# Optimization experiments

Measured on AMD Instinct MI355X. Metric: run time of the kernel, lower is better.

Reference implementation:

```python
import jax, jax.numpy as jnp
import numpy as np
import math

NUM_HEADS = 16
D_MODEL = 1024
BATCH = 1
SEQ_LEN = 4096


def alibi_slopes(num_heads):
    # slopes m_h = (256 ** (1/H)) ** -(h+1)
    x = (2.0 ** 8) ** (1.0 / num_heads)
    return jnp.asarray([1.0 / x ** (i + 1) for i in range(num_heads)], dtype=jnp.float32)


def setup_inputs() -> dict:
    key = jax.random.key(0)
    k1, k2 = jax.random.split(key)
    x = jax.random.normal(k1, (BATCH, SEQ_LEN, D_MODEL), dtype=jnp.float32)
    # nn.Linear(d_model, 3*d_model, bias=False); store as [d_model, 3*d_model] so y = x @ w
    w_kqv = jax.random.normal(k2, (D_MODEL, 3 * D_MODEL), dtype=jnp.float32) * (1.0 / math.sqrt(D_MODEL))
    return {"x": x, "w_kqv": w_kqv}


def reference(x, w_kqv):
    B, S, D = x.shape
    H = NUM_HEADS
    dh = D // H
    scale = jnp.asarray(math.sqrt(D), dtype=x.dtype)  # module divides by sqrt(d_model)

    kqv = x @ w_kqv  # [B, S, 3D]
    # NOTE: original chunks as (key, query, value) in that order
    k, q, v = jnp.split(kqv, 3, axis=-1)
    q = q.reshape(B, S, H, dh)
    k = k.reshape(B, S, H, dh)
    v = v.reshape(B, S, H, dh)

    # ALiBi bias: m_h * (j - i), shape [H, S, S]
    pos = jnp.arange(S)
    rel = pos[None, :] - pos[:, None]  # [S, S], x - y
    slopes = alibi_slopes(H).astype(x.dtype)  # [H]
    bias = slopes[:, None, None] * rel.astype(x.dtype)  # [H, S, S]

    score = jnp.einsum('bihd,bjhd->bhij', q, k) / scale + bias[None]  # [B, H, S, S]
    causal = rel <= 0  # j <= i (lower triangular)
    score = jnp.where(causal[None, None], score, jnp.asarray(-jnp.inf, dtype=score.dtype))

    attn = jax.nn.softmax(score, axis=-1)
    out = jnp.einsum('bhij,bjhd->bihd', attn, v).reshape(B, S, D)
    return out
```

## Files before the change

kernel.cpp:

```cpp
#include <hip/hip_runtime.h>
#include <stdint.h>
#include <math.h>

#define SEQ 4096
#define DM  1024
#define NH  16
#define DH  64
#define PPAD 72
#define LOG2E 1.44269504088896341f

typedef short bf16x8 __attribute__((ext_vector_type(8)));
typedef short bf16x4 __attribute__((ext_vector_type(4)));
typedef float f32x4  __attribute__((ext_vector_type(4)));

typedef const __attribute__((address_space(1))) short* gptr_t;
typedef __attribute__((address_space(3))) short* lptr_t;

__device__ __forceinline__ short f2bf(float f) {
    union { float f; uint32_t u; } x; x.f = f;
    uint32_t r = (x.u + 0x7fffu + ((x.u >> 16) & 1u)) >> 16;
    return (short)r;
}
__device__ __forceinline__ short f2bf_trunc(float f) {
    union { float f; uint32_t u; } x; x.f = f;
    return (short)(x.u >> 16);
}

__device__ __forceinline__ void load_lds16(const short* g, const short* l) {
    __builtin_amdgcn_global_load_lds((gptr_t)(uintptr_t)g,
                                     (lptr_t)(uint32_t)(uintptr_t)l, 16, 0, 0);
}

__global__ __launch_bounds__(256) void cvt_fused(const float* __restrict__ x,
                                                 const float* __restrict__ w,
                                                 short* __restrict__ xb,
                                                 short* __restrict__ wtb) {
    __shared__ float T[64][69];
    const int b = blockIdx.x;
    if (b < 2048) {
        const int i = (b * 256 + threadIdx.x) * 8;
        float4 a0 = ((const float4*)(x + i))[0];
        float4 a1 = ((const float4*)(x + i))[1];
        bf16x8 p;
        p[0]=f2bf(a0.x); p[1]=f2bf(a0.y); p[2]=f2bf(a0.z); p[3]=f2bf(a0.w);
        p[4]=f2bf(a1.x); p[5]=f2bf(a1.y); p[6]=f2bf(a1.z); p[7]=f2bf(a1.w);
        *(bf16x8*)(xb + i) = p;
        return;
    }
    const int bb = b - 2048;
    const int n0 = (bb % 48) * 64, k0 = (bb / 48) * 64;
    const int t = threadIdx.x;
    {
        const int kr = t >> 4, nc = (t & 15) * 4;
        #pragma unroll
        for (int i = 0; i < 4; ++i) {
            float4 v = *(const float4*)(w + (size_t)(k0 + kr + i * 16) * 3072 + n0 + nc);
            T[kr + i * 16][nc + 0] = v.x; T[kr + i * 16][nc + 1] = v.y;
            T[kr + i * 16][nc + 2] = v.z; T[kr + i * 16][nc + 3] = v.w;
        }
    }
    __syncthreads();
    const int nr = t >> 4, kc = (t & 15) * 4;
    #pragma unroll
    for (int i = 0; i < 4; ++i) {
        const int n = n0 + nr + i * 16;
        const float sc = (n >= 1024 && n < 2048) ? (LOG2E / 32.0f) : 1.0f;
        short4 o;
        o.x = f2bf(T[kc + 0][nr + i * 16] * sc);
        o.y = f2bf(T[kc + 1][nr + i * 16] * sc);
        o.z = f2bf(T[kc + 2][nr + i * 16] * sc);
        o.w = f2bf(T[kc + 3][nr + i * 16] * sc);
        *(short4*)(wtb + (size_t)n * 1024 + k0 + kc) = o;
    }
}

__global__ __launch_bounds__(256) void qkv_gemm(const short* __restrict__ xb,
                                                const short* __restrict__ wtb,
                                                short* __restrict__ kq,
                                                short* __restrict__ vt) {
    __shared__ short As[128 * 64];
    __shared__ short Bs[128 * 64];
    const int col0 = blockIdx.y * 128, row0 = blockIdx.x * 128;
    const int tid = threadIdx.x, w = tid >> 6, lane = tid & 63;
    const int lmod = lane & 15, ldiv = lane >> 4;
    const int wr = (w >> 1) * 64, wc = (w & 1) * 64;

    f32x4 acc[4][4] = {};
    const short* Ag = xb  + (size_t)row0 * DM;
    const short* Bg = wtb + (size_t)col0 * DM;

    for (int k0 = 0; k0 < DM; k0 += 64) {
        __syncthreads();
        #pragma unroll
        for (int t = 0; t < 4; ++t) {
            const int o = (w * 4 + t) * 1024 + lane * 16;
            const int r = o >> 7, cs = (o & 127) >> 1;
            load_lds16(Ag + (size_t)r * DM + k0 + cs, As + (w * 4 + t) * 512);
            load_lds16(Bg + (size_t)r * DM + k0 + cs, Bs + (w * 4 + t) * 512);
        }
        __syncthreads();
        #pragma unroll
        for (int ks = 0; ks < 2; ++ks) {
            bf16x8 af[4], bf[4];
            #pragma unroll
            for (int i = 0; i < 4; ++i)
                af[i] = *(const bf16x8*)(As + (wr + i * 16 + lmod) * 64 + ks * 32 + ldiv * 8);
            #pragma unroll
            for (int j = 0; j < 4; ++j)
                bf[j] = *(const bf16x8*)(Bs + (wc + j * 16 + lmod) * 64 + ks * 32 + ldiv * 8);
            #pragma unroll
            for (int i = 0; i < 4; ++i)
                #pragma unroll
                for (int j = 0; j < 4; ++j)
                    acc[i][j] = __builtin_amdgcn_mfma_f32_16x16x32_bf16(af[i], bf[j], acc[i][j], 0, 0, 0);
        }
    }

    if (col0 < 2048) {
        #pragma unroll
        for (int i = 0; i < 4; ++i)
            #pragma unroll
            for (int j = 0; j < 4; ++j)
                #pragma unroll
                for (int r = 0; r < 4; ++r)
                    kq[(size_t)(row0 + wr + i * 16 + ldiv * 4 + r) * 2048
                       + col0 + wc + j * 16 + lmod] = f2bf(acc[i][j][r]);
    } else {
        #pragma unroll
        for (int i = 0; i < 4; ++i) {
            const int ig = row0 + wr + i * 16 + ldiv * 4;
            #pragma unroll
            for (int j = 0; j < 4; ++j) {
                const int cg = col0 + wc + j * 16 + lmod - 2048;
                const int h = cg >> 6, d = cg & 63;
                bf16x4 p;
                p[0]=f2bf(acc[i][j][0]); p[1]=f2bf(acc[i][j][1]);
                p[2]=f2bf(acc[i][j][2]); p[3]=f2bf(acc[i][j][3]);
                *(bf16x4*)(vt + (size_t)(h * 64 + d) * SEQ + ig) = p;
            }
        }
    }
}

__global__ __launch_bounds__(256, 4) void attn(const short* __restrict__ kq,
                                               const short* __restrict__ vt,
                                               float* __restrict__ o0,
                                               float* __restrict__ o1,
                                               float* __restrict__ ls0,
                                               float* __restrict__ ls1) {
    __shared__ short Ks[64 * 64];
    __shared__ short Vs[64 * 64];
    __shared__ short Ps[4 * 32 * PPAD];

    const int b = blockIdx.x;
    const int band = b >> 8, pos = b & 255, g = pos >> 5;
    const int qt = (band & 1) ? (24 - band * 8 + g) : (31 - band * 8 - g);
    const int h = (pos >> 1) & 15, s = pos & 1;

    const int tid = threadIdx.x, w = tid >> 6, lane = tid & 63;
    const int lmod = lane & 15, ldiv = lane >> 4;
    const float slope2 = exp2f(-0.5f * (float)(h + 1)) * LOG2E;

    const int sr0 = w * 16 + (lane >> 3), sr1 = sr0 + 8;
    const int sc0 = (lane & 7) ^ (sr0 & 7), sc1 = (lane & 7) ^ (sr1 & 7);

    const int xorm = lmod & 7;
    const int cx0 = ldiv ^ xorm;
    const int cx1 = (4 + ldiv) ^ xorm;
    const int rowbase = qt * 128 + w * 32;
    short* pw = Ps + w * 32 * PPAD;

    bf16x8 qf[2][2];
    #pragma unroll
    for (int m = 0; m < 2; ++m) {
        const short* qp = kq + (size_t)(rowbase + m * 16 + lmod) * 2048 + 1024 + h * 64;
        qf[m][0] = *(const bf16x8*)(qp + ldiv * 8);
        qf[m][1] = *(const bf16x8*)(qp + 32 + ldiv * 8);
    }
    int db[2];
    float pre[2][4];
    #pragma unroll
    for (int m = 0; m < 2; ++m) {
        db[m] = lmod - (rowbase + m * 16 + ldiv * 4);
        #pragma unroll
        for (int r = 0; r < 4; ++r) pre[m][r] = slope2 * (float)(db[m] - r);
    }

    f32x4 O[2][4] = {};
    float lsum[2][4] = {};
    const int kt0 = s ? (qt + 1) : 0;
    const int kt1 = s ? (2 * qt + 2) : (qt + 1);

    for (int kt = kt0; kt < kt1; ++kt) {
        __syncthreads();
        {
            const short* kb = kq + (size_t)(kt * 64) * 2048 + h * 64;
            load_lds16(kb + (size_t)sr0 * 2048 + sc0 * 8, Ks + (w * 16) * 64);
            load_lds16(kb + (size_t)sr1 * 2048 + sc1 * 8, Ks + (w * 16 + 8) * 64);
            const short* vb = vt + (size_t)(h * 64) * SEQ + kt * 64;
            load_lds16(vb + (size_t)sr0 * SEQ + sc0 * 8, Vs + (w * 16) * 64);
            load_lds16(vb + (size_t)sr1 * SEQ + sc1 * 8, Vs + (w * 16 + 8) * 64);
        }
        __syncthreads();

        const bool diag = (kt >= 2 * qt);
        const float cb = slope2 * (float)(kt * 64);
        const int dt = kt * 64;

        #pragma unroll
        for (int nt = 0; nt < 4; ++nt) {
            const float cn = cb + slope2 * (float)(nt * 16);
            f32x4 sc[2];
            #pragma unroll
            for (int m = 0; m < 2; ++m)
                #pragma unroll
                for (int r = 0; r < 4; ++r) sc[m][r] = pre[m][r] + cn;
            #pragma unroll
            for (int ks = 0; ks < 2; ++ks) {
                bf16x8 kf = *(const bf16x8*)(Ks + (nt * 16 + lmod) * 64 + ((ks ? cx1 : cx0) << 3));
                #pragma unroll
                for (int m = 0; m < 2; ++m)
                    sc[m] = __builtin_amdgcn_mfma_f32_16x16x32_bf16(qf[m][ks], kf, sc[m], 0, 0, 0);
            }
            if (diag) {
                #pragma unroll
                for (int m = 0; m < 2; ++m)
                    #pragma unroll
                    for (int r = 0; r < 4; ++r) {
                        float v = sc[m][r];
                        if (dt + nt * 16 - r + db[m] > 0) v = -1e30f;
                        const float p = __builtin_amdgcn_exp2f(v);
                        lsum[m][r] += p;
                        pw[(m * 16 + ldiv * 4 + r) * PPAD + nt * 16 + lmod] = f2bf_trunc(p);
                    }
            } else {
                #pragma unroll
                for (int m = 0; m < 2; ++m)
                    #pragma unroll
                    for (int r = 0; r < 4; ++r) {
                        const float p = __builtin_amdgcn_exp2f(sc[m][r]);
                        lsum[m][r] += p;
                        pw[(m * 16 + ldiv * 4 + r) * PPAD + nt * 16 + lmod] = f2bf_trunc(p);
                    }
            }
        }

        bf16x8 pa[2][2];
        #pragma unroll
        for (int m = 0; m < 2; ++m) {
            pa[m][0] = *(const bf16x8*)(pw + (m * 16 + lmod) * PPAD + ldiv * 8);
            pa[m][1] = *(const bf16x8*)(pw + (m * 16 + lmod) * PPAD + 32 + ldiv * 8);
        }
        #pragma unroll
        for (int ks = 0; ks < 2; ++ks) {
            const int cxo = (ks ? cx1 : cx0) << 3;
            #pragma unroll
            for (int nt = 0; nt < 4; ++nt) {
                bf16x8 vf = *(const bf16x8*)(Vs + (nt * 16 + lmod) * 64 + cxo);
                #pragma unroll
                for (int m = 0; m < 2; ++m)
                    O[m][nt] = __builtin_amdgcn_mfma_f32_16x16x32_bf16(pa[m][ks], vf, O[m][nt], 0, 0, 0);
            }
        }
    }

    #pragma unroll
    for (int m = 0; m < 2; ++m)
        #pragma unroll
        for (int r = 0; r < 4; ++r) {
            float v = lsum[m][r];
            v += __shfl_xor(v, 1, 16);
            v += __shfl_xor(v, 2, 16);
            v += __shfl_xor(v, 4, 16);
            v += __shfl_xor(v, 8, 16);
            lsum[m][r] = v;
        }

    float* ob = s ? o1 : o0;
    float* lb = s ? ls1 : ls0;
    #pragma unroll
    for (int m = 0; m < 2; ++m) {
        const int i0 = rowbase + m * 16 + ldiv * 4;
        #pragma unroll
        for (int nt = 0; nt < 4; ++nt)
            #pragma unroll
            for (int r = 0; r < 4; ++r)
                ob[(size_t)(i0 + r) * DM + h * 64 + nt * 16 + lmod] = O[m][nt][r];
    }
    if (lmod == 0) {
        #pragma unroll
        for (int m = 0; m < 2; ++m)
            #pragma unroll
            for (int r = 0; r < 4; ++r)
                lb[h * SEQ + rowbase + m * 16 + ldiv * 4 + r] = lsum[m][r];
    }
}

__global__ __launch_bounds__(256) void combine(float* __restrict__ out,
                                               const float* __restrict__ opart,
                                               const float* __restrict__ ls0,
                                               const float* __restrict__ ls1) {
    const int i8 = (blockIdx.x * 256 + threadIdx.x) * 8;
    const int row = i8 >> 10, col = i8 & 1023, h = col >> 6;
    const float l = ls0[h * SEQ + row] + ls1[h * SEQ + row];
    const float rc = 1.0f / l;
    float4 a0 = *(const float4*)(out + i8);
    float4 a1 = *(const float4*)(out + i8 + 4);
    float4 b0 = *(const float4*)(opart + i8);
    float4 b1 = *(const float4*)(opart + i8 + 4);
    float4 c0, c1;
    c0.x = (a0.x + b0.x) * rc; c0.y = (a0.y + b0.y) * rc;
    c0.z = (a0.z + b0.z) * rc; c0.w = (a0.w + b0.w) * rc;
    c1.x = (a1.x + b1.x) * rc; c1.y = (a1.y + b1.y) * rc;
    c1.z = (a1.z + b1.z) * rc; c1.w = (a1.w + b1.w) * rc;
    *(float4*)(out + i8) = c0;
    *(float4*)(out + i8 + 4) = c1;
}

extern "C" void kernel_launch(void* const* d_in, const int* in_sizes, int n_in,
                              void* d_out, int out_size, void* d_ws, size_t ws_size,
                              hipStream_t stream) {
    const float* x = (const float*)d_in[0];
    const float* w = (const float*)d_in[1];
    float* out = (float*)d_out;

    char* ws = (char*)d_ws;
    short* kq    = (short*)(ws);
    short* vt    = (short*)(ws + ((size_t)16 << 20));
    short* xb    = (short*)(ws + ((size_t)24 << 20));
    short* wtb   = (short*)(ws + ((size_t)32 << 20));
    float* opart = (float*)(ws + ((size_t)24 << 20));
    float* ls0   = (float*)(ws + ((size_t)40 << 20));
    float* ls1   = (float*)(ws + ((size_t)40 << 20) + (256 << 10));

    cvt_fused<<<2048 + 768, 256, 0, stream>>>(x, w, xb, wtb);
    qkv_gemm <<<dim3(SEQ / 128, 3072 / 128), 256, 0, stream>>>(xb, wtb, kq, vt);
    attn     <<<1024, 256, 0, stream>>>(kq, vt, out, opart, ls0, ls1);
    combine  <<<SEQ * DM / (256 * 8), 256, 0, stream>>>(out, opart, ls0, ls1);
}
```

Measured before the change: 191.3 us.

## Keep P in registers via transposed QK MFMA and double-buffer K/V tiles

```diff
diff --git a/kernel.cpp b/kernel.cpp
--- a/kernel.cpp
+++ b/kernel.cpp
@@ -6,12 +6,12 @@
 #define DM  1024
 #define NH  16
 #define DH  64
-#define PPAD 72
 #define LOG2E 1.44269504088896341f
 
 typedef short bf16x8 __attribute__((ext_vector_type(8)));
 typedef short bf16x4 __attribute__((ext_vector_type(4)));
 typedef float f32x4  __attribute__((ext_vector_type(4)));
+typedef uint32_t u32x4 __attribute__((ext_vector_type(4)));
 
 typedef const __attribute__((address_space(1))) short* gptr_t;
 typedef __attribute__((address_space(3))) short* lptr_t;
@@ -21,14 +21,18 @@
     uint32_t r = (x.u + 0x7fffu + ((x.u >> 16) & 1u)) >> 16;
     return (short)r;
 }
-__device__ __forceinline__ short f2bf_trunc(float f) {
-    union { float f; uint32_t u; } x; x.f = f;
-    return (short)(x.u >> 16);
+__device__ __forceinline__ uint32_t pkbf(float lo, float hi) {
+    union { float f; uint32_t u; } a, b; a.f = lo; b.f = hi;
+    return (a.u >> 16) | (b.u & 0xffff0000u);
 }
 
 __device__ __forceinline__ void load_lds16(const short* g, const short* l) {
     __builtin_amdgcn_global_load_lds((gptr_t)(uintptr_t)g,
                                      (lptr_t)(uint32_t)(uintptr_t)l, 16, 0, 0);
+}
+__device__ __forceinline__ void load_lds4(const short* g, const short* l) {
+    __builtin_amdgcn_global_load_lds((gptr_t)(uintptr_t)g,
+                                     (lptr_t)(uint32_t)(uintptr_t)l, 4, 0, 0);
 }
 
 __global__ __launch_bounds__(256) void cvt_fused(const float* __restrict__ x,
@@ -148,9 +152,8 @@
                                                float* __restrict__ o1,
                                                float* __restrict__ ls0,
                                                float* __restrict__ ls1) {
-    __shared__ short Ks[64 * 64];
-    __shared__ short Vs[64 * 64];
-    __shared__ short Ps[4 * 32 * PPAD];
+    __shared__ short Ks[2][64 * 64];
+    __shared__ short Vs[2][64 * 64];
 
     const int b = blockIdx.x;
     const int band = b >> 8, pos = b & 255, g = pos >> 5;
@@ -164,11 +167,20 @@
     const int sr0 = w * 16 + (lane >> 3), sr1 = sr0 + 8;
     const int sc0 = (lane & 7) ^ (sr0 & 7), sc1 = (lane & 7) ^ (sr1 & 7);
 
+    const int dd = lane >> 5, cphys = (lane >> 2) & 7, uu = lane & 3;
+    int voff[8];
+    #pragma unroll
+    for (int i = 0; i < 8; ++i) {
+        const int d = w * 16 + i * 2 + dd;
+        const int lc = cphys ^ (d & 7);
+        const int kkg = (lc >> 2) * 32 + (uu >> 1) * 16 + (lc & 3) * 4 + (uu & 1) * 2;
+        voff[i] = d * SEQ + kkg;
+    }
+
     const int xorm = lmod & 7;
-    const int cx0 = ldiv ^ xorm;
-    const int cx1 = (4 + ldiv) ^ xorm;
+    const int cxs0 = (ldiv ^ xorm) * 8;
+    const int cxs1 = ((4 + ldiv) ^ xorm) * 8;
     const int rowbase = qt * 128 + w * 32;
-    short* pw = Ps + w * 32 * PPAD;
 
     bf16x8 qf[2][2];
     #pragma unroll
@@ -177,104 +189,107 @@
         qf[m][0] = *(const bf16x8*)(qp + ldiv * 8);
         qf[m][1] = *(const bf16x8*)(qp + 32 + ldiv * 8);
     }
-    int db[2];
+    int db2[2];
     float pre[2][4];
     #pragma unroll
     for (int m = 0; m < 2; ++m) {
-        db[m] = lmod - (rowbase + m * 16 + ldiv * 4);
-        #pragma unroll
-        for (int r = 0; r < 4; ++r) pre[m][r] = slope2 * (float)(db[m] - r);
+        db2[m] = 4 * ldiv - (rowbase + m * 16 + lmod);
+        #pragma unroll
+        for (int r = 0; r < 4; ++r) pre[m][r] = slope2 * (float)(db2[m] + r);
     }
 
     f32x4 O[2][4] = {};
-    float lsum[2][4] = {};
+    float lsum[2] = {};
     const int kt0 = s ? (qt + 1) : 0;
     const int kt1 = s ? (2 * qt + 2) : (qt + 1);
 
+    auto stage = [&](int kt_, int bsel) {
+        short* Kb = (short*)Ks[bsel];
+        short* Vb = (short*)Vs[bsel];
+        const short* kb = kq + (size_t)(kt_ * 64) * 2048 + h * 64;
+        load_lds16(kb + (size_t)sr0 * 2048 + sc0 * 8, Kb + (w * 16) * 64);
+        load_lds16(kb + (size_t)sr1 * 2048 + sc1 * 8, Kb + (w * 16 + 8) * 64);
+        const short* vb = vt + (size_t)(h * 64) * SEQ + kt_ * 64;
+        #pragma unroll
+        for (int i = 0; i < 8; ++i)
+            load_lds4(vb + voff[i], Vb + (w * 16 + i * 2) * 64);
+    };
+
+    int cur = 0;
+    stage(kt0, 0);
+    __syncthreads();
+
     for (int kt = kt0; kt < kt1; ++kt) {
-        __syncthreads();
-        {
-            const short* kb = kq + (size_t)(kt * 64) * 2048 + h * 64;
-            load_lds16(kb + (size_t)sr0 * 2048 + sc0 * 8, Ks + (w * 16) * 64);
-            load_lds16(kb + (size_t)sr1 * 2048 + sc1 * 8, Ks + (w * 16 + 8) * 64);
-            const short* vb = vt + (size_t)(h * 64) * SEQ + kt * 64;
-            load_lds16(vb + (size_t)sr0 * SEQ + sc0 * 8, Vs + (w * 16) * 64);
-            load_lds16(vb + (size_t)sr1 * SEQ + sc1 * 8, Vs + (w * 16 + 8) * 64);
-        }
-        __syncthreads();
-
+        if (kt + 1 < kt1) stage(kt + 1, cur ^ 1);
+
+        const short* Kb = (const short*)Ks[cur];
+        const short* Vb = (const short*)Vs[cur];
         const bool diag = (kt >= 2 * qt);
-        const float cb = slope2 * (float)(kt * 64);
         const int dt = kt * 64;
-
-        #pragma unroll
-        for (int nt = 0; nt < 4; ++nt) {
-            const float cn = cb + slope2 * (float)(nt * 16);
-            f32x4 sc[2];
-            #pragma unroll
-            for (int m = 0; m < 2; ++m)
+        const float cb = slope2 * (float)dt;
+
+        #pragma unroll
+        for (int ks = 0; ks < 2; ++ks) {
+            u32x4 pk0, pk1;
+            #pragma unroll
+            for (int j1 = 0; j1 < 2; ++j1) {
+                const int nt = ks * 2 + j1;
+                const float cn = cb + slope2 * (float)(nt * 16);
+                f32x4 s0, s1;
                 #pragma unroll
-                for (int r = 0; r < 4; ++r) sc[m][r] = pre[m][r] + cn;
-            #pragma unroll
-            for (int ks = 0; ks < 2; ++ks) {
-                bf16x8 kf = *(const bf16x8*)(Ks + (nt * 16 + lmod) * 64 + ((ks ? cx1 : cx0) << 3));
-                #pragma unroll
-                for (int m = 0; m < 2; ++m)
-                    sc[m] = __builtin_amdgcn_mfma_f32_16x16x32_bf16(qf[m][ks], kf, sc[m], 0, 0, 0);
-            }
-            if (diag) {
-                #pragma unroll
-                for (int m = 0; m < 2; ++m)
+                for (int r = 0; r < 4; ++r) { s0[r] = pre[0][r] + cn; s1[r] = pre[1][r] + cn; }
+                const bf16x8 kf0 = *(const bf16x8*)(Kb + (nt * 16 + lmod) * 64 + cxs0);
+                const bf16x8 kf1 = *(const bf16x8*)(Kb + (nt * 16 + lmod) * 64 + cxs1);
+                s0 = __builtin_amdgcn_mfma_f32_16x16x32_bf16(kf0, qf[0][0], s0, 0, 0, 0);
+                s0 = __builtin_amdgcn_mfma_f32_16x16x32_bf16(kf1, qf[0][1], s0, 0, 0, 0);
+                s1 = __builtin_amdgcn_mfma_f32_16x16x32_bf16(kf0, qf[1][0], s1, 0, 0, 0);
+                s1 = __builtin_amdgcn_mfma_f32_16x16x32_bf16(kf1, qf[1][1], s1, 0, 0, 0);
+
+                float p0[4], p1[4];
+                if (diag) {
                     #pragma unroll
                     for (int r = 0; r < 4; ++r) {
-                        float v = sc[m][r];
-                        if (dt + nt * 16 - r + db[m] > 0) v = -1e30f;
-                        const float p = __builtin_amdgcn_exp2f(v);
-                        lsum[m][r] += p;
-                        pw[(m * 16 + ldiv * 4 + r) * PPAD + nt * 16 + lmod] = f2bf_trunc(p);
+                        float v0 = s0[r], v1 = s1[r];
+                        if (dt + nt * 16 + r + db2[0] > 0) v0 = -1e30f;
+                        if (dt + nt * 16 + r + db2[1] > 0) v1 = -1e30f;
+                        p0[r] = __builtin_amdgcn_exp2f(v0);
+                        p1[r] = __builtin_amdgcn_exp2f(v1);
                     }
-            } else {
-                #pragma unroll
-                for (int m = 0; m < 2; ++m)
+                } else {
                     #pragma unroll
                     for (int r = 0; r < 4; ++r) {
-                        const float p = __builtin_amdgcn_exp2f(sc[m][r]);
-                        lsum[m][r] += p;
-                        pw[(m * 16 + ldiv * 4 + r) * PPAD + nt * 16 + lmod] = f2bf_trunc(p);
+                        p0[r] = __builtin_amdgcn_exp2f(s0[r]);
+                        p1[r] = __builtin_amdgcn_exp2f(s1[r]);
                     }
+                }
+                lsum[0] += (p0[0] + p0[1]) + (p0[2] + p0[3]);
+                lsum[1] += (p1[0] + p1[1]) + (p1[2] + p1[3]);
+                pk0[j1 * 2]     = pkbf(p0[0], p0[1]);
+                pk0[j1 * 2 + 1] = pkbf(p0[2], p0[3]);
+                pk1[j1 * 2]     = pkbf(p1[0], p1[1]);
+                pk1[j1 * 2 + 1] = pkbf(p1[2], p1[3]);
             }
-        }
-
-        bf16x8 pa[2][2];
-        #pragma unroll
-        for (int m = 0; m < 2; ++m) {
-            pa[m][0] = *(const bf16x8*)(pw + (m * 16 + lmod) * PPAD + ldiv * 8);
-            pa[m][1] = *(const bf16x8*)(pw + (m * 16 + lmod) * PPAD + 32 + ldiv * 8);
-        }
-        #pragma unroll
-        for (int ks = 0; ks < 2; ++ks) {
-            const int cxo = (ks ? cx1 : cx0) << 3;
-            #pragma unroll
-            for (int nt = 0; nt < 4; ++nt) {
-                bf16x8 vf = *(const bf16x8*)(Vs + (nt * 16 + lmod) * 64 + cxo);
-                #pragma unroll
-                for (int m = 0; m < 2; ++m)
-                    O[m][nt] = __builtin_amdgcn_mfma_f32_16x16x32_bf16(pa[m][ks], vf, O[m][nt], 0, 0, 0);
+            const bf16x8 pa0 = __builtin_bit_cast(bf16x8, pk0);
+            const bf16x8 pa1 = __builtin_bit_cast(bf16x8, pk1);
+            const int cxo = ks ? cxs1 : cxs0;
+            #pragma unroll
+            for (int nt2 = 0; nt2 < 4; ++nt2) {
+                const bf16x8 vf = *(const bf16x8*)(Vb + (nt2 * 16 + lmod) * 64 + cxo);
+                O[0][nt2] = __builtin_amdgcn_mfma_f32_16x16x32_bf16(pa0, vf, O[0][nt2], 0, 0, 0);
+                O[1][nt2] = __builtin_amdgcn_mfma_f32_16x16x32_bf16(pa1, vf, O[1][nt2], 0, 0, 0);
             }
         }
-    }
-
-    #pragma unroll
-    for (int m = 0; m < 2; ++m)
-        #pragma unroll
-        for (int r = 0; r < 4; ++r) {
-            float v = lsum[m][r];
-            v += __shfl_xor(v, 1, 16);
-            v += __shfl_xor(v, 2, 16);
-            v += __shfl_xor(v, 4, 16);
-            v += __shfl_xor(v, 8, 16);
-            lsum[m][r] = v;
-        }
+        __syncthreads();
+        cur ^= 1;
+    }
+
+    #pragma unroll
+    for (int m = 0; m < 2; ++m) {
+        float v = lsum[m];
+        v += __shfl_xor(v, 16);
+        v += __shfl_xor(v, 32);
+        lsum[m] = v;
+    }
 
     float* ob = s ? o1 : o0;
     float* lb = s ? ls1 : ls0;
@@ -282,17 +297,15 @@
     for (int m = 0; m < 2; ++m) {
         const int i0 = rowbase + m * 16 + ldiv * 4;
         #pragma unroll
-        for (int nt = 0; nt < 4; ++nt)
+        for (int nt2 = 0; nt2 < 4; ++nt2)
             #pragma unroll
             for (int r = 0; r < 4; ++r)
-                ob[(size_t)(i0 + r) * DM + h * 64 + nt * 16 + lmod] = O[m][nt][r];
-    }
-    if (lmod == 0) {
+                ob[(size_t)(i0 + r) * DM + h * 64 + nt2 * 16 + lmod] = O[m][nt2][r];
+    }
+    if (ldiv == 0) {
         #pragma unroll
         for (int m = 0; m < 2; ++m)
-            #pragma unroll
-            for (int r = 0; r < 4; ++r)
-                lb[h * SEQ + rowbase + m * 16 + ldiv * 4 + r] = lsum[m][r];
+            lb[h * SEQ + rowbase + m * 16 + lmod] = lsum[m];
     }
 }
 
```

Result: slower. 207.6 us (+8.5%).
